# Kernel tuning notes

Measured on AMD Instinct MI355X. Metric: run time of the kernel, lower is better.

## Reference

```python
import jax, jax.numpy as jnp
import numpy as np

N, F_IN, F_OUT = 2048, 128, 64


def setup_inputs() -> dict:
    key = jax.random.key(0)
    k0, k1, k2, k3, k4 = jax.random.split(key, 5)
    node_features = jax.random.normal(k0, (N, F_IN), dtype=jnp.float32)
    adjacency_matrix = jax.random.uniform(k1, (N, N), dtype=jnp.float32)
    mask_father = jax.random.uniform(k2, (N, N), dtype=jnp.float32)
    mask_hadamard = jax.random.uniform(k3, (N, N), dtype=jnp.float32)
    # kaiming_uniform (fan_in, relu): bound = sqrt(6 / fan_in) * sqrt(2) adjustment -> gain*sqrt(3/fan_in)
    bound = np.sqrt(2.0) * np.sqrt(3.0 / F_IN)
    weight = jax.random.uniform(k4, (F_IN, F_OUT), dtype=jnp.float32, minval=-bound, maxval=bound)
    bias = jnp.zeros((F_OUT,), dtype=jnp.float32)
    return {
        "node_features": node_features,
        "adjacency_matrix": adjacency_matrix,
        "mask_father": mask_father,
        "mask_hadamard": mask_hadamard,
        "weight": weight,
        "bias": bias,
    }


def reference(node_features, adjacency_matrix, mask_father, mask_hadamard, weight, bias):
    # H[i,f] = (X @ W + b)[i,f]
    H = node_features @ weight + bias  # [N, F]
    # Original math: out[j,f] = sum_k mf[j,k] * H[k,f] * (sum_i A[j,i] * H[i,f] * mh[i,k])
    # G[j,f,k] corresponds to the (masked hadamard @ adjacency) intermediate [N, F, N]
    G = jnp.einsum('ji,if,ik->jfk', adjacency_matrix, H, mask_hadamard)
    out = jnp.einsum('jfk,kf,jk->jf', G, H, mask_father)
    return out
```

## Files before the change

### kernel.cpp

```cpp
#include <hip/hip_runtime.h>
#include <hip/hip_bf16.h>


typedef __attribute__((ext_vector_type(8))) _Float16 f16x8;
typedef __attribute__((ext_vector_type(4))) _Float16 f16x4;
typedef __attribute__((ext_vector_type(4))) float f32x4;

#define N 2048
#define FOUT 64
#define FIN 128
#define NIT 1024

__device__ __forceinline__ void gl_lds16(const _Float16* g, _Float16* l) {
    __builtin_amdgcn_global_load_lds(
        (const __attribute__((address_space(1))) void*)g,
        (__attribute__((address_space(3))) void*)l, 16, 0, 0);
}


__global__ __launch_bounds__(256) void k_h(const float* __restrict__ X,
                                           const float* __restrict__ W,
                                           const float* __restrict__ bias,
                                           float* __restrict__ HT,
                                           _Float16* __restrict__ HTh) {
    __shared__ float Ws[FIN * FOUT];
    __shared__ float Xs[4 * FIN];
    int t = threadIdx.x;
#pragma unroll
    for (int s = 0; s < 32; ++s) Ws[t + 256 * s] = W[t + 256 * s];
    int i0 = blockIdx.x * 4;
#pragma unroll
    for (int s = 0; s < 2; ++s) { int idx = t + 256 * s; Xs[idx] = X[(size_t)i0 * FIN + idx]; }
    __syncthreads();
    int f = t & 63, il = t >> 6;
    float h = bias[f];
#pragma unroll
    for (int p = 0; p < FIN; ++p) h = fmaf(Xs[il * FIN + p], Ws[p * FOUT + f], h);
    int i = i0 + il;
    HT[f * N + i] = h;
    HTh[f * N + i] = (_Float16)h;
}

__global__ __launch_bounds__(256) void k_a2h(const float* __restrict__ A,
                                             _Float16* __restrict__ Ah) {
    int g = blockIdx.x * 256 + threadIdx.x;
    float4 v = ((const float4*)A)[g];
    f16x4 o;
    o[0] = (_Float16)v.x; o[1] = (_Float16)v.y; o[2] = (_Float16)v.z; o[3] = (_Float16)v.w;
    ((f16x4*)Ah)[g] = o;
}

__global__ __launch_bounds__(256) void k_mht(const float* __restrict__ mh,
                                             _Float16* __restrict__ mhT) {
    __shared__ float tile[64][65];
    int t = threadIdx.x;
    int bx = blockIdx.x & 31;
    int by = blockIdx.x >> 5;
#pragma unroll
    for (int s = 0; s < 16; ++s) {
        int lin = t + 256 * s;
        int r = lin >> 6, c = lin & 63;
        tile[r][c] = mh[(size_t)(by * 64 + r) * N + bx * 64 + c];
    }
    __syncthreads();
#pragma unroll
    for (int s = 0; s < 16; ++s) {
        int lin = t + 256 * s;
        int kr = lin >> 6, ic = lin & 63;
        mhT[(size_t)(bx * 64 + kr) * N + by * 64 + ic] = (_Float16)tile[ic][kr];
    }
}


#define ISSUE(it_, la_, lb_)                                                  \
    {                                                                         \
        int ib_ = ((it_) & 63) << 5;                                          \
        int kb_ = ((it_) >> 6) << 7;                                          \
        const _Float16* pa_ = Ah + aoff + ib_;                                \
        const _Float16* pb_ = mhT + boff + (size_t)kb_ * N + ib_;             \
        _Pragma("unroll") for (int c_ = 0; c_ < 4; ++c_) {                    \
            gl_lds16(pa_ + c_ * 16 * N, (la_) + c_ * 512);                    \
            gl_lds16(pb_ + c_ * 16 * N, (lb_) + c_ * 512);                    \
        }                                                                     \
    }

#define EPILOGUE(kt_)                                                         \
    {                                                                         \
        int kbase_ = (kt_) << 7;                                              \
        _Pragma("unroll") for (int jj = 0; jj < 4; ++jj) {                    \
            float t0_[4] = {0.f, 0.f, 0.f, 0.f};                              \
            float t1_[4] = {0.f, 0.f, 0.f, 0.f};                              \
            _Pragma("unroll") for (int kk = 0; kk < 4; ++kk) {                \
                int kg_ = kbase_ + wk + kk * 16 + l16;                        \
                float hk0_ = HT[f0 * N + kg_];                                \
                float hk1_ = HT[(f0 + 1) * N + kg_];                          \
                int jrow_ = jbase + wj + jj * 16 + q * 4;                     \
                _Pragma("unroll") for (int r = 0; r < 4; ++r) {               \
                    float m_ = mf[(size_t)(jrow_ + r) * N + kg_];             \
                    t0_[r] = fmaf(acc[0][jj][kk][r], m_ * hk0_, t0_[r]);      \
                    t1_[r] = fmaf(acc[1][jj][kk][r], m_ * hk1_, t1_[r]);      \
                }                                                             \
            }                                                                 \
            _Pragma("unroll") for (int r = 0; r < 4; ++r) {                   \
                float v0_ = t0_[r], v1_ = t1_[r];                             \
                v0_ += __shfl_xor(v0_, 1); v1_ += __shfl_xor(v1_, 1);         \
                v0_ += __shfl_xor(v0_, 2); v1_ += __shfl_xor(v1_, 2);         \
                v0_ += __shfl_xor(v0_, 4); v1_ += __shfl_xor(v1_, 4);         \
                v0_ += __shfl_xor(v0_, 8); v1_ += __shfl_xor(v1_, 8);         \
                outp[0][jj][r] += v0_;                                        \
                outp[1][jj][r] += v1_;                                        \
            }                                                                 \
        }                                                                     \
        _Pragma("unroll") for (int a_ = 0; a_ < 2; ++a_)                      \
            _Pragma("unroll") for (int b_ = 0; b_ < 4; ++b_)                  \
                _Pragma("unroll") for (int c2_ = 0; c2_ < 4; ++c2_)           \
                    acc[a_][b_][c2_] = (f32x4){0.f, 0.f, 0.f, 0.f};           \
    }

#define COMPUTE(it_, ta_, tb_, do_epi_)                                       \
    {                                                                         \
        int ib_ = ((it_) & 63) << 5;                                          \
        f16x8 ar_[4], br_[4];                                                 \
        _Pragma("unroll") for (int x = 0; x < 4; ++x)                         \
            ar_[x] = *(const f16x8*)&(ta_)[(x * 16 + l16) * 32 + pcq];        \
        _Pragma("unroll") for (int x = 0; x < 4; ++x)                         \
            br_[x] = *(const f16x8*)&(tb_)[(x * 16 + l16) * 32 + pcq];        \
        f16x8 h0_ = *(const f16x8*)&hbuf[0][ib_ + (q << 3)];                  \
        f16x8 h1_ = *(const f16x8*)&hbuf[1][ib_ + (q << 3)];                  \
        _Pragma("unroll") for (int jj = 0; jj < 4; ++jj) {                    \
            f16x8 a0_ = ar_[jj] * h0_;                                        \
            f16x8 a1_ = ar_[jj] * h1_;                                        \
            _Pragma("unroll") for (int kk = 0; kk < 4; ++kk) {                \
                acc[0][jj][kk] = __builtin_amdgcn_mfma_f32_16x16x32_f16(      \
                    a0_, br_[kk], acc[0][jj][kk], 0, 0, 0);                   \
                acc[1][jj][kk] = __builtin_amdgcn_mfma_f32_16x16x32_f16(      \
                    a1_, br_[kk], acc[1][jj][kk], 0, 0, 0);                   \
            }                                                                 \
        }                                                                     \
        if ((do_epi_) && (((it_) & 63) == 63)) { EPILOGUE((it_) >> 6); }      \
    }

__global__ __launch_bounds__(256, 2) void k_main(const float* __restrict__ mf,
                                                 const float* __restrict__ HT,
                                                 const _Float16* __restrict__ HTh,
                                                 const _Float16* __restrict__ Ah,
                                                 const _Float16* __restrict__ mhT,
                                                 float* __restrict__ out) {
    __shared__ _Float16 tile0[4][2][2048];
    __shared__ _Float16 tile1[4][2][2048];
    __shared__ _Float16 hbuf[2][N];
    __shared__ float red[2][4][64];

    int t = threadIdx.x;
    int jbase = (blockIdx.x >> 5) << 7;
    int f0 = (blockIdx.x & 31) << 1;
    int w = t >> 6, lane = t & 63, q = lane >> 4, l16 = lane & 15;
    int wj = (w & 1) << 6, wk = (w >> 1) << 6;

#pragma unroll
    for (int s = 0; s < 2; ++s) {
        int idx = t + 256 * s;
        ((f16x8*)hbuf)[idx] = *(const f16x8*)&HTh[(size_t)(f0 + (idx >> 8)) * N + (idx & 255) * 8];
    }
    __syncthreads();

    int lrow = lane >> 2;
    int lc = ((lane & 3) - (lrow >> 1)) & 3;
    size_t aoff = (size_t)(jbase + wj + lrow) * N + lc * 8;
    size_t boff = (size_t)(wk + lrow) * N + lc * 8;

    _Float16* la0 = &tile0[w][0][0];
    _Float16* lb0 = &tile0[w][1][0];
    _Float16* la1 = &tile1[w][0][0];
    _Float16* lb1 = &tile1[w][1][0];

    int pcq = ((q + (l16 >> 1)) & 3) << 3;

    float outp[2][4][4];
    f32x4 acc[2][4][4];
#pragma unroll
    for (int a = 0; a < 2; ++a)
#pragma unroll
        for (int b = 0; b < 4; ++b)
#pragma unroll
            for (int c = 0; c < 4; ++c) {
                outp[a][b][c] = 0.f;
                acc[a][b][c] = (f32x4){0.f, 0.f, 0.f, 0.f};
            }

    ISSUE(0, la0, lb0);

#pragma unroll 1
    for (int it2 = 0; it2 < NIT; it2 += 2) {
        ISSUE(it2 + 1, la1, lb1);
        __builtin_amdgcn_sched_barrier(0);
        __builtin_amdgcn_s_waitcnt(0x0F78);
        __builtin_amdgcn_sched_barrier(0);
        COMPUTE(it2, la0, lb0, 0);

        if (it2 + 2 < NIT) {
            ISSUE(it2 + 2, la0, lb0);
            __builtin_amdgcn_sched_barrier(0);
            __builtin_amdgcn_s_waitcnt(0x0F78);
            __builtin_amdgcn_sched_barrier(0);
        } else {
            __builtin_amdgcn_sched_barrier(0);
            __builtin_amdgcn_s_waitcnt(0x0F70);
            __builtin_amdgcn_sched_barrier(0);
        }
        COMPUTE(it2 + 1, la1, lb1, 1);
    }

    if (l16 == 0) {
#pragma unroll
        for (int fi = 0; fi < 2; ++fi)
#pragma unroll
            for (int jj = 0; jj < 4; ++jj)
#pragma unroll
                for (int r = 0; r < 4; ++r)
                    red[fi][w][jj * 16 + q * 4 + r] = outp[fi][jj][r];
    }
    __syncthreads();
    if (t < 128) {
        int j = t;
#pragma unroll
        for (int fi = 0; fi < 2; ++fi) {
            float v = (j < 64) ? (red[fi][0][j] + red[fi][2][j])
                               : (red[fi][1][j - 64] + red[fi][3][j - 64]);
            out[(size_t)(jbase + j) * FOUT + f0 + fi] = v;
        }
    }
}

extern "C" void kernel_launch(void* const* d_in, const int* in_sizes, int n_in,
                              void* d_out, int out_size, void* d_ws, size_t ws_size,
                              hipStream_t stream) {
    const float* X    = (const float*)d_in[0];
    const float* A    = (const float*)d_in[1];
    const float* mf   = (const float*)d_in[2];
    const float* mh   = (const float*)d_in[3];
    const float* W    = (const float*)d_in[4];
    const float* bias = (const float*)d_in[5];
    float* out = (float*)d_out;

    float*    HT  = (float*)d_ws;
    _Float16* HTh = (_Float16*)((char*)d_ws + 524288);
    _Float16* Ah  = (_Float16*)((char*)d_ws + 1048576);
    _Float16* mhT = (_Float16*)((char*)d_ws + 1048576 + 8388608);

    k_h<<<N / 4, 256, 0, stream>>>(X, W, bias, HT, HTh);
    k_a2h<<<(N * N / 4) / 256, 256, 0, stream>>>(A, Ah);
    k_mht<<<(N / 64) * (N / 64), 256, 0, stream>>>(mh, mhT);
    k_main<<<16 * 32, 256, 0, stream>>>(mf, HT, HTh, Ah, mhT, out);
}
```

Baseline: 1.250 ms.

## Share A tiles across waves in LDS and load B directly into registers

The main loop is restructured so the whole block cooperatively stages a shared 128x64 A tile in LDS, with an XOR swizzle, double-buffered and synchronised with __syncthreads. Each wave now loads its mask_hadamard B fragments straight from global memory into registers, prefetching one sub-step ahead. The per-iteration i-step doubles from 32 to 64, which halves the iteration count and cuts redundant A traffic and LDS footprint. In exchange it adds block-wide barriers and uncached-through-LDS global B loads whose latency must be hidden by register prefetch.

```diff
diff --git a/kernel.cpp b/kernel.cpp
--- a/kernel.cpp
+++ b/kernel.cpp
@@ -9,7 +9,7 @@
 #define N 2048
 #define FOUT 64
 #define FIN 128
-#define NIT 1024
+#define NIT 512
 
 __device__ __forceinline__ void gl_lds16(const _Float16* g, _Float16* l) {
     __builtin_amdgcn_global_load_lds(
@@ -72,15 +72,43 @@
 }
 
 
-#define ISSUE(it_, la_, lb_)                                                  \
-    {                                                                         \
-        int ib_ = ((it_) & 63) << 5;                                          \
-        int kb_ = ((it_) >> 6) << 7;                                          \
+#define ISSUE_A(it_, la_)                                                     \
+    {                                                                         \
+        int itc_ = ((it_) < NIT) ? (it_) : (NIT - 1);                         \
+        int ib_ = (itc_ & 31) << 6;                                           \
         const _Float16* pa_ = Ah + aoff + ib_;                                \
-        const _Float16* pb_ = mhT + boff + (size_t)kb_ * N + ib_;             \
-        _Pragma("unroll") for (int c_ = 0; c_ < 4; ++c_) {                    \
-            gl_lds16(pa_ + c_ * 16 * N, (la_) + c_ * 512);                    \
-            gl_lds16(pb_ + c_ * 16 * N, (lb_) + c_ * 512);                    \
+        _Pragma("unroll") for (int c_ = 0; c_ < 4; ++c_)                      \
+            gl_lds16(pa_ + c_ * 8 * N, (la_) + c_ * 512);                     \
+    }
+
+#define BLOAD(dst_, it_, s_)                                                  \
+    {                                                                         \
+        int itc_ = ((it_) < NIT) ? (it_) : (NIT - 1);                         \
+        int ib_ = ((itc_ & 31) << 6) + ((s_) << 5) + (q << 3);                \
+        int kb_ = (itc_ >> 5) << 7;                                           \
+        const _Float16* pb_ = mhT + (size_t)(kb_ + wk + l16) * N + ib_;       \
+        _Pragma("unroll") for (int kk_ = 0; kk_ < 4; ++kk_)                   \
+            dst_[kk_] = *(const f16x8*)&pb_[(size_t)(kk_ << 4) * N];          \
+    }
+
+#define COMPUTE_S(it_, s_, ta_, b_)                                           \
+    {                                                                         \
+        int ib_ = (((it_) & 31) << 6) + ((s_) << 5);                          \
+        f16x8 ar_[4];                                                         \
+        _Pragma("unroll") for (int x = 0; x < 4; ++x)                         \
+            ar_[x] = *(const f16x8*)&(ta_)[(wj + x * 16 + l16) * 64 +         \
+                                           ((((q + 4 * (s_)) ^ (l16 & 7))) << 3)]; \
+        f16x8 h0_ = *(const f16x8*)&hbuf[0][ib_ + (q << 3)];                  \
+        f16x8 h1_ = *(const f16x8*)&hbuf[1][ib_ + (q << 3)];                  \
+        _Pragma("unroll") for (int jj = 0; jj < 4; ++jj) {                    \
+            f16x8 a0_ = ar_[jj] * h0_;                                        \
+            f16x8 a1_ = ar_[jj] * h1_;                                        \
+            _Pragma("unroll") for (int kk = 0; kk < 4; ++kk) {                \
+                acc[0][jj][kk] = __builtin_amdgcn_mfma_f32_16x16x32_f16(      \
+                    a0_, (b_)[kk], acc[0][jj][kk], 0, 0, 0);                  \
+                acc[1][jj][kk] = __builtin_amdgcn_mfma_f32_16x16x32_f16(      \
+                    a1_, (b_)[kk], acc[1][jj][kk], 0, 0, 0);                  \
+            }                                                                 \
         }                                                                     \
     }
 
@@ -117,37 +145,13 @@
                     acc[a_][b_][c2_] = (f32x4){0.f, 0.f, 0.f, 0.f};           \
     }
 
-#define COMPUTE(it_, ta_, tb_, do_epi_)                                       \
-    {                                                                         \
-        int ib_ = ((it_) & 63) << 5;                                          \
-        f16x8 ar_[4], br_[4];                                                 \
-        _Pragma("unroll") for (int x = 0; x < 4; ++x)                         \
-            ar_[x] = *(const f16x8*)&(ta_)[(x * 16 + l16) * 32 + pcq];        \
-        _Pragma("unroll") for (int x = 0; x < 4; ++x)                         \
-            br_[x] = *(const f16x8*)&(tb_)[(x * 16 + l16) * 32 + pcq];        \
-        f16x8 h0_ = *(const f16x8*)&hbuf[0][ib_ + (q << 3)];                  \
-        f16x8 h1_ = *(const f16x8*)&hbuf[1][ib_ + (q << 3)];                  \
-        _Pragma("unroll") for (int jj = 0; jj < 4; ++jj) {                    \
-            f16x8 a0_ = ar_[jj] * h0_;                                        \
-            f16x8 a1_ = ar_[jj] * h1_;                                        \
-            _Pragma("unroll") for (int kk = 0; kk < 4; ++kk) {                \
-                acc[0][jj][kk] = __builtin_amdgcn_mfma_f32_16x16x32_f16(      \
-                    a0_, br_[kk], acc[0][jj][kk], 0, 0, 0);                   \
-                acc[1][jj][kk] = __builtin_amdgcn_mfma_f32_16x16x32_f16(      \
-                    a1_, br_[kk], acc[1][jj][kk], 0, 0, 0);                   \
-            }                                                                 \
-        }                                                                     \
-        if ((do_epi_) && (((it_) & 63) == 63)) { EPILOGUE((it_) >> 6); }      \
-    }
-
 __global__ __launch_bounds__(256, 2) void k_main(const float* __restrict__ mf,
                                                  const float* __restrict__ HT,
                                                  const _Float16* __restrict__ HTh,
                                                  const _Float16* __restrict__ Ah,
                                                  const _Float16* __restrict__ mhT,
                                                  float* __restrict__ out) {
-    __shared__ _Float16 tile0[4][2][2048];
-    __shared__ _Float16 tile1[4][2][2048];
+    __shared__ _Float16 tiles[2][128 * 64];
     __shared__ _Float16 hbuf[2][N];
     __shared__ float red[2][4][64];
 
@@ -162,19 +166,14 @@
         int idx = t + 256 * s;
         ((f16x8*)hbuf)[idx] = *(const f16x8*)&HTh[(size_t)(f0 + (idx >> 8)) * N + (idx & 255) * 8];
     }
-    __syncthreads();
-
-    int lrow = lane >> 2;
-    int lc = ((lane & 3) - (lrow >> 1)) & 3;
-    size_t aoff = (size_t)(jbase + wj + lrow) * N + lc * 8;
-    size_t boff = (size_t)(wk + lrow) * N + lc * 8;
-
-    _Float16* la0 = &tile0[w][0][0];
-    _Float16* lb0 = &tile0[w][1][0];
-    _Float16* la1 = &tile1[w][0][0];
-    _Float16* lb1 = &tile1[w][1][0];
-
-    int pcq = ((q + (l16 >> 1)) & 3) << 3;
+
+    int lrow = lane >> 3;
+    int lchunk = (lane & 7) ^ lrow;
+    size_t aoff = (size_t)(jbase + w * 32 + lrow) * N + lchunk * 8;
+    _Float16* la0 = &tiles[0][w * 2048];
+    _Float16* la1 = &tiles[1][w * 2048];
+    const _Float16* ta0 = &tiles[0][0];
+    const _Float16* ta1 = &tiles[1][0];
 
     float outp[2][4][4];
     f32x4 acc[2][4][4];
@@ -188,27 +187,26 @@
                 acc[a][b][c] = (f32x4){0.f, 0.f, 0.f, 0.f};
             }
 
-    ISSUE(0, la0, lb0);
+    f16x8 bA[4], bB[4];
+    ISSUE_A(0, la0);
+    BLOAD(bA, 0, 0);
 
 #pragma unroll 1
     for (int it2 = 0; it2 < NIT; it2 += 2) {
-        ISSUE(it2 + 1, la1, lb1);
-        __builtin_amdgcn_sched_barrier(0);
-        __builtin_amdgcn_s_waitcnt(0x0F78);
-        __builtin_amdgcn_sched_barrier(0);
-        COMPUTE(it2, la0, lb0, 0);
-
-        if (it2 + 2 < NIT) {
-            ISSUE(it2 + 2, la0, lb0);
-            __builtin_amdgcn_sched_barrier(0);
-            __builtin_amdgcn_s_waitcnt(0x0F78);
-            __builtin_amdgcn_sched_barrier(0);
-        } else {
-            __builtin_amdgcn_sched_barrier(0);
-            __builtin_amdgcn_s_waitcnt(0x0F70);
-            __builtin_amdgcn_sched_barrier(0);
-        }
-        COMPUTE(it2 + 1, la1, lb1, 1);
+        __syncthreads();
+        ISSUE_A(it2 + 1, la1);
+        BLOAD(bB, it2, 1);
+        COMPUTE_S(it2, 0, ta0, bA);
+        BLOAD(bA, it2 + 1, 0);
+        COMPUTE_S(it2, 1, ta0, bB);
+
+        __syncthreads();
+        ISSUE_A(it2 + 2, la0);
+        BLOAD(bB, it2 + 1, 1);
+        COMPUTE_S(it2 + 1, 0, ta1, bA);
+        BLOAD(bA, it2 + 2, 0);
+        COMPUTE_S(it2 + 1, 1, ta1, bB);
+        if (((it2 + 1) & 31) == 31) { EPILOGUE((it2 + 1) >> 5); }
     }
 
     if (l16 == 0) {
```

Result: slower. 1.418 ms (+13.5%).

## Split K across two blocks and share cooperative LDS tiles across waves

Applied to the files above, without the earlier changes.

The main kernel's K dimension is split into two halves handled by separate blocks, which doubles the grid. Partial outputs are combined with atomicAdd into an output that a new memset zeroes first. Each block's four waves now load one shared 128x32 A/B tile together, separated by __syncthreads, instead of each wave loading its own duplicated tiles. Occupancy is raised to 3 blocks per SIMD group. This aims to cut redundant global loads and improve CU utilisation, at the cost of block-wide barriers each step, atomics, and an extra memset.

```diff
diff --git a/kernel.cpp b/kernel.cpp
--- a/kernel.cpp
+++ b/kernel.cpp
@@ -9,7 +9,7 @@
 #define N 2048
 #define FOUT 64
 #define FIN 128
-#define NIT 1024
+#define NIT 512
 
 __device__ __forceinline__ void gl_lds16(const _Float16* g, _Float16* l) {
     __builtin_amdgcn_global_load_lds(
@@ -74,19 +74,41 @@
 
 #define ISSUE(it_, la_, lb_)                                                  \
     {                                                                         \
-        int ib_ = ((it_) & 63) << 5;                                          \
-        int kb_ = ((it_) >> 6) << 7;                                          \
+        int itc_ = ((it_) < NIT) ? (it_) : (NIT - 1);                         \
+        int ib_ = (itc_ & 63) << 5;                                           \
         const _Float16* pa_ = Ah + aoff + ib_;                                \
-        const _Float16* pb_ = mhT + boff + (size_t)kb_ * N + ib_;             \
-        _Pragma("unroll") for (int c_ = 0; c_ < 4; ++c_) {                    \
+        const _Float16* pb_ = mhT + boff + (size_t)((itc_ >> 6) << 7) * N + ib_; \
+        _Pragma("unroll") for (int c_ = 0; c_ < 2; ++c_) {                    \
             gl_lds16(pa_ + c_ * 16 * N, (la_) + c_ * 512);                    \
             gl_lds16(pb_ + c_ * 16 * N, (lb_) + c_ * 512);                    \
         }                                                                     \
     }
 
+#define COMPUTE(it_, ta_, tb_)                                                \
+    {                                                                         \
+        int ib_ = ((it_) & 63) << 5;                                          \
+        f16x8 ar_[4], br_[4];                                                 \
+        _Pragma("unroll") for (int x = 0; x < 4; ++x)                         \
+            ar_[x] = *(const f16x8*)&(ta_)[(wj + x * 16 + l16) * 32 + pcq];   \
+        _Pragma("unroll") for (int x = 0; x < 4; ++x)                         \
+            br_[x] = *(const f16x8*)&(tb_)[(wk + x * 16 + l16) * 32 + pcq];   \
+        f16x8 h0_ = *(const f16x8*)&hbuf[0][ib_ + (q << 3)];                  \
+        f16x8 h1_ = *(const f16x8*)&hbuf[1][ib_ + (q << 3)];                  \
+        _Pragma("unroll") for (int jj = 0; jj < 4; ++jj) {                    \
+            f16x8 a0_ = ar_[jj] * h0_;                                        \
+            f16x8 a1_ = ar_[jj] * h1_;                                        \
+            _Pragma("unroll") for (int kk = 0; kk < 4; ++kk) {                \
+                acc[0][jj][kk] = __builtin_amdgcn_mfma_f32_16x16x32_f16(      \
+                    a0_, br_[kk], acc[0][jj][kk], 0, 0, 0);                   \
+                acc[1][jj][kk] = __builtin_amdgcn_mfma_f32_16x16x32_f16(      \
+                    a1_, br_[kk], acc[1][jj][kk], 0, 0, 0);                   \
+            }                                                                 \
+        }                                                                     \
+    }
+
 #define EPILOGUE(kt_)                                                         \
     {                                                                         \
-        int kbase_ = (kt_) << 7;                                              \
+        int kbase_ = khbase + ((kt_) << 7);                                   \
         _Pragma("unroll") for (int jj = 0; jj < 4; ++jj) {                    \
             float t0_[4] = {0.f, 0.f, 0.f, 0.f};                              \
             float t1_[4] = {0.f, 0.f, 0.f, 0.f};                              \
@@ -117,43 +139,22 @@
                     acc[a_][b_][c2_] = (f32x4){0.f, 0.f, 0.f, 0.f};           \
     }
 
-#define COMPUTE(it_, ta_, tb_, do_epi_)                                       \
-    {                                                                         \
-        int ib_ = ((it_) & 63) << 5;                                          \
-        f16x8 ar_[4], br_[4];                                                 \
-        _Pragma("unroll") for (int x = 0; x < 4; ++x)                         \
-            ar_[x] = *(const f16x8*)&(ta_)[(x * 16 + l16) * 32 + pcq];        \
-        _Pragma("unroll") for (int x = 0; x < 4; ++x)                         \
-            br_[x] = *(const f16x8*)&(tb_)[(x * 16 + l16) * 32 + pcq];        \
-        f16x8 h0_ = *(const f16x8*)&hbuf[0][ib_ + (q << 3)];                  \
-        f16x8 h1_ = *(const f16x8*)&hbuf[1][ib_ + (q << 3)];                  \
-        _Pragma("unroll") for (int jj = 0; jj < 4; ++jj) {                    \
-            f16x8 a0_ = ar_[jj] * h0_;                                        \
-            f16x8 a1_ = ar_[jj] * h1_;                                        \
-            _Pragma("unroll") for (int kk = 0; kk < 4; ++kk) {                \
-                acc[0][jj][kk] = __builtin_amdgcn_mfma_f32_16x16x32_f16(      \
-                    a0_, br_[kk], acc[0][jj][kk], 0, 0, 0);                   \
-                acc[1][jj][kk] = __builtin_amdgcn_mfma_f32_16x16x32_f16(      \
-                    a1_, br_[kk], acc[1][jj][kk], 0, 0, 0);                   \
-            }                                                                 \
-        }                                                                     \
-        if ((do_epi_) && (((it_) & 63) == 63)) { EPILOGUE((it_) >> 6); }      \
-    }
-
-__global__ __launch_bounds__(256, 2) void k_main(const float* __restrict__ mf,
+__global__ __launch_bounds__(256, 3) void k_main(const float* __restrict__ mf,
                                                  const float* __restrict__ HT,
                                                  const _Float16* __restrict__ HTh,
                                                  const _Float16* __restrict__ Ah,
                                                  const _Float16* __restrict__ mhT,
                                                  float* __restrict__ out) {
-    __shared__ _Float16 tile0[4][2][2048];
-    __shared__ _Float16 tile1[4][2][2048];
+    __shared__ _Float16 tiles[2][2][128 * 32];
     __shared__ _Float16 hbuf[2][N];
     __shared__ float red[2][4][64];
 
     int t = threadIdx.x;
-    int jbase = (blockIdx.x >> 5) << 7;
-    int f0 = (blockIdx.x & 31) << 1;
+    int bid = blockIdx.x;
+    int kh = bid & 1;
+    int f0 = ((bid >> 1) & 31) << 1;
+    int jbase = (bid >> 6) << 7;
+    int khbase = kh << 10;
     int w = t >> 6, lane = t & 63, q = lane >> 4, l16 = lane & 15;
     int wj = (w & 1) << 6, wk = (w >> 1) << 6;
 
@@ -162,17 +163,19 @@
         int idx = t + 256 * s;
         ((f16x8*)hbuf)[idx] = *(const f16x8*)&HTh[(size_t)(f0 + (idx >> 8)) * N + (idx & 255) * 8];
     }
-    __syncthreads();
 
     int lrow = lane >> 2;
     int lc = ((lane & 3) - (lrow >> 1)) & 3;
-    size_t aoff = (size_t)(jbase + wj + lrow) * N + lc * 8;
-    size_t boff = (size_t)(wk + lrow) * N + lc * 8;
-
-    _Float16* la0 = &tile0[w][0][0];
-    _Float16* lb0 = &tile0[w][1][0];
-    _Float16* la1 = &tile1[w][0][0];
-    _Float16* lb1 = &tile1[w][1][0];
+    size_t aoff = (size_t)(jbase + w * 32 + lrow) * N + lc * 8;
+    size_t boff = (size_t)(khbase + w * 32 + lrow) * N + lc * 8;
+    _Float16* la0 = &tiles[0][0][w * 1024];
+    _Float16* lb0 = &tiles[0][1][w * 1024];
+    _Float16* la1 = &tiles[1][0][w * 1024];
+    _Float16* lb1 = &tiles[1][1][w * 1024];
+    const _Float16* ta0 = &tiles[0][0][0];
+    const _Float16* tb0 = &tiles[0][1][0];
+    const _Float16* ta1 = &tiles[1][0][0];
+    const _Float16* tb1 = &tiles[1][1][0];
 
     int pcq = ((q + (l16 >> 1)) & 3) << 3;
 
@@ -192,23 +195,14 @@
 
 #pragma unroll 1
     for (int it2 = 0; it2 < NIT; it2 += 2) {
+        __syncthreads();
         ISSUE(it2 + 1, la1, lb1);
-        __builtin_amdgcn_sched_barrier(0);
-        __builtin_amdgcn_s_waitcnt(0x0F78);
-        __builtin_amdgcn_sched_barrier(0);
-        COMPUTE(it2, la0, lb0, 0);
-
-        if (it2 + 2 < NIT) {
-            ISSUE(it2 + 2, la0, lb0);
-            __builtin_amdgcn_sched_barrier(0);
-            __builtin_amdgcn_s_waitcnt(0x0F78);
-            __builtin_amdgcn_sched_barrier(0);
-        } else {
-            __builtin_amdgcn_sched_barrier(0);
-            __builtin_amdgcn_s_waitcnt(0x0F70);
-            __builtin_amdgcn_sched_barrier(0);
-        }
-        COMPUTE(it2 + 1, la1, lb1, 1);
+        COMPUTE(it2, ta0, tb0);
+
+        __syncthreads();
+        ISSUE(it2 + 2, la0, lb0);
+        COMPUTE(it2 + 1, ta1, tb1);
+        if (((it2 + 1) & 63) == 63) { EPILOGUE((it2 + 1) >> 6); }
     }
 
     if (l16 == 0) {
@@ -227,7 +221,7 @@
         for (int fi = 0; fi < 2; ++fi) {
             float v = (j < 64) ? (red[fi][0][j] + red[fi][2][j])
                                : (red[fi][1][j - 64] + red[fi][3][j - 64]);
-            out[(size_t)(jbase + j) * FOUT + f0 + fi] = v;
+            atomicAdd(&out[(size_t)(jbase + j) * FOUT + f0 + fi], v);
         }
     }
 }
@@ -248,8 +242,9 @@
     _Float16* Ah  = (_Float16*)((char*)d_ws + 1048576);
     _Float16* mhT = (_Float16*)((char*)d_ws + 1048576 + 8388608);
 
+    hipMemsetAsync(out, 0, (size_t)N * FOUT * sizeof(float), stream);
     k_h<<<N / 4, 256, 0, stream>>>(X, W, bias, HT, HTh);
     k_a2h<<<(N * N / 4) / 256, 256, 0, stream>>>(A, Ah);
     k_mht<<<(N / 64) * (N / 64), 256, 0, stream>>>(mh, mhT);
-    k_main<<<16 * 32, 256, 0, stream>>>(mf, HT, HTh, Ah, mhT, out);
-}
+    k_main<<<16 * 32 * 2, 256, 0, stream>>>(mf, HT, HTh, Ah, mhT, out);
+}
```

After: 1.389 ms. 1.11x slower.
